# Performance work log

Measured on AMD Instinct MI355X. Metric: run time of the kernel, lower is better.

## Reference

```python
import jax, jax.numpy as jnp
import numpy as np

N = 50000   # nodes
E = 600000  # edges
D = 128     # in = hidden = out channels (must be equal per the cat/mean readout)
B = 4096    # number of lookup indices


def setup_inputs() -> dict:
    key = jax.random.key(0)
    ks = jax.random.split(key, 8)
    x = jax.random.normal(ks[0], (N, D), dtype=jnp.float32)
    edge_index = jax.random.randint(ks[1], (2, E), 0, N)
    edge_weight = jax.random.uniform(ks[2], (E,), dtype=jnp.float32)
    inputs_idx = jax.random.randint(ks[3], (B,), 0, N + 1)  # N is the appended zero row
    def lin_w(k, din, dout):
        return jax.random.normal(k, (din, dout), dtype=jnp.float32) / np.sqrt(din).astype(np.float32)
    W1 = lin_w(ks[4], D, D); b1 = jnp.zeros((D,), jnp.float32)
    W2 = lin_w(ks[5], D, D); b2 = jnp.zeros((D,), jnp.float32)
    W3 = lin_w(ks[6], D, D); b3 = jnp.zeros((D,), jnp.float32)
    return {"inputs_idx": inputs_idx, "x": x, "edge_index": edge_index,
            "edge_weight": edge_weight, "W1": W1, "b1": b1, "W2": W2,
            "b2": b2, "W3": W3, "b3": b3}


def gcn_conv(x, W, b, src, dst, w):
    # PyG GCNConv with add_self_loops=True (fill weight 1) and symmetric norm.
    deg = jnp.zeros((N,), x.dtype).at[dst].add(w) + 1.0  # self-loop contributes 1
    dinv = jax.lax.rsqrt(deg)
    norm = dinv[src] * w * dinv[dst]                      # [E]
    h = x @ W                                             # [N, D]
    agg = jax.ops.segment_sum(norm[:, None] * h[src], dst, num_segments=N)
    agg = agg + h * (dinv * dinv)[:, None]                # self-loop term: deg^-1 * h
    return agg + b


def lookup(x, inputs_idx):
    # append a zero row, then gather
    x_ = jnp.concatenate([x, jnp.zeros((1, x.shape[-1]), x.dtype)], axis=0)
    return x_[inputs_idx]  # [B, D]


def reference(inputs_idx, x, edge_index, edge_weight, W1, b1, W2, b2, W3, b3):
    src, dst = edge_index[0], edge_index[1]
    x1 = jax.nn.relu(gcn_conv(x, W1, b1, src, dst, edge_weight))
    x2 = jax.nn.relu(gcn_conv(x1, W2, b2, src, dst, edge_weight))
    x3 = jax.nn.relu(gcn_conv(x2, W3, b3, src, dst, edge_weight))
    e1 = lookup(x1, inputs_idx)
    e2 = lookup(x2, inputs_idx)
    e3 = lookup(x3, inputs_idx)
    # torch.cat([1,B,D]x3, dim=0).mean(0) == elementwise mean of the three
    return (e1 + e2 + e3) / 3.0
```

## Files before the change

### kernel.cpp

```cpp
#include <hip/hip_runtime.h>
#include <hip/hip_fp16.h>

#define D 128
#define STRIDE 48

typedef _Float16 f16x8 __attribute__((ext_vector_type(8)));
typedef float f32x4 __attribute__((ext_vector_type(4)));
struct h4 { __half2 a, b; };

__global__ __launch_bounds__(256) void zero_kernel(int* __restrict__ p, int n) {
  int i = blockIdx.x * 256 + threadIdx.x;
  if (i < n) p[i] = 0;
}

__global__ __launch_bounds__(256) void build_kernel(
    const int* __restrict__ ei, const float* __restrict__ ew,
    int* __restrict__ cnt, int2* __restrict__ pairs, int E) {
  int e = blockIdx.x * 256 + threadIdx.x;
  if (e >= E) return;
  int s = ei[e], d = ei[E + e];
  int rank = atomicAdd(&cnt[d], 1);
  if (rank < STRIDE) pairs[(size_t)d * STRIDE + rank] = make_int2(s, __float_as_int(ew[e]));
}

__global__ __launch_bounds__(256) void deg_dinv_kernel(
    int* __restrict__ cnt, const int2* __restrict__ pairs,
    float* __restrict__ dinv, int N) {
  int n = blockIdx.x * 4 + (threadIdx.x >> 6);
  int lane = threadIdx.x & 63;
  if (n >= N) return;
  int c = cnt[n];
  c = c < STRIDE ? c : STRIDE;
  float v = (lane < c) ? __int_as_float(pairs[(size_t)n * STRIDE + lane].y) : 0.f;
#pragma unroll
  for (int o = 32; o > 0; o >>= 1) v += __shfl_xor(v, o, 64);
  if (lane == 0) {
    dinv[n] = rsqrtf(v + 1.0f);
    cnt[n] = c;
  }
}

__global__ __launch_bounds__(256) void norm_kernel(
    const int* __restrict__ cnt, const float* __restrict__ dinv,
    int2* __restrict__ pairs, int N) {
  int n = blockIdx.x * 4 + (threadIdx.x >> 6);
  int lane = threadIdx.x & 63;
  if (n >= N) return;
  int c = cnt[n];
  float di = dinv[n];
  if (lane < c) {
    int2 p = pairs[(size_t)n * STRIDE + lane];
    p.y = __float_as_int(dinv[p.x] * __int_as_float(p.y) * di);
    pairs[(size_t)n * STRIDE + lane] = p;
  }
}

__global__ __launch_bounds__(256) void tohalf_kernel(
    const float* __restrict__ in, __half* __restrict__ out, int n4) {
  int t = blockIdx.x * 256 + threadIdx.x;
  if (t >= n4) return;
  float4 v = ((const float4*)in)[t];
  h4 o = {__floats2half2_rn(v.x, v.y), __floats2half2_rn(v.z, v.w)};
  ((h4*)out)[t] = o;
}

__global__ __launch_bounds__(256) void wtrans_kernel(
    const float* __restrict__ W1, const float* __restrict__ W2,
    const float* __restrict__ W3, __half* __restrict__ WT1,
    __half* __restrict__ WT2, __half* __restrict__ WT3) {
  int t = blockIdx.x * 256 + threadIdx.x;
  if (t >= 3 * D * D) return;
  int m = t >> 14;
  int i = t & (D * D - 1);
  int k = i >> 7, n = i & 127;
  const float* W = (m == 0) ? W1 : (m == 1) ? W2 : W3;
  __half* WT = (m == 0) ? WT1 : (m == 1) ? WT2 : WT3;
  WT[n * D + k] = __float2half(W[k * D + n]);
}

__global__ __launch_bounds__(256) void agg_kernel(
    const __half* __restrict__ x16, const float* __restrict__ dinv,
    const int* __restrict__ cnt, const int2* __restrict__ pairs,
    __half* __restrict__ agg16, int N) {
  int gw = (blockIdx.x * 256 + threadIdx.x) >> 6;
  int lane = threadIdx.x & 63;
  if (gw >= N) return;
  const __half2* xs = (const __half2*)x16;
  float di = dinv[gw];
  int c = cnt[gw];
  const int2* pr = pairs + (size_t)gw * STRIDE;
  float2 acc = __half22float2(xs[(size_t)gw * 64 + lane]);
  acc.x *= di * di;
  acc.y *= di * di;
  int e = 0;
  for (; e + 4 <= c; e += 4) {
    int2 p0 = pr[e], p1 = pr[e + 1], p2 = pr[e + 2], p3 = pr[e + 3];
    float n0 = __int_as_float(p0.y), n1 = __int_as_float(p1.y);
    float n2 = __int_as_float(p2.y), n3 = __int_as_float(p3.y);
    float2 v0 = __half22float2(xs[(size_t)p0.x * 64 + lane]);
    float2 v1 = __half22float2(xs[(size_t)p1.x * 64 + lane]);
    float2 v2 = __half22float2(xs[(size_t)p2.x * 64 + lane]);
    float2 v3 = __half22float2(xs[(size_t)p3.x * 64 + lane]);
    acc.x += n0 * v0.x + n1 * v1.x + n2 * v2.x + n3 * v3.x;
    acc.y += n0 * v0.y + n1 * v1.y + n2 * v2.y + n3 * v3.y;
  }
  for (; e < c; e++) {
    int2 p0 = pr[e];
    float n0 = __int_as_float(p0.y);
    float2 v0 = __half22float2(xs[(size_t)p0.x * 64 + lane]);
    acc.x += n0 * v0.x;
    acc.y += n0 * v0.y;
  }
  ((__half2*)agg16)[(size_t)gw * 64 + lane] = __floats2half2_rn(acc.x, acc.y);
}

__global__ __launch_bounds__(256) void agg_idx_kernel(
    const __half* __restrict__ x16, const float* __restrict__ dinv,
    const int* __restrict__ cnt, const int2* __restrict__ pairs,
    const int* __restrict__ idx, __half* __restrict__ aggI, int B, int N) {
  int gw = (blockIdx.x * 256 + threadIdx.x) >> 6;
  int lane = threadIdx.x & 63;
  if (gw >= B) return;
  const __half2* xs = (const __half2*)x16;
  float2 acc = make_float2(0.f, 0.f);
  int node = idx[gw];
  if ((unsigned)node < (unsigned)N) {
    float di = dinv[node];
    int c = cnt[node];
    const int2* pr = pairs + (size_t)node * STRIDE;
    acc = __half22float2(xs[(size_t)node * 64 + lane]);
    acc.x *= di * di;
    acc.y *= di * di;
    int e = 0;
    for (; e + 4 <= c; e += 4) {
      int2 p0 = pr[e], p1 = pr[e + 1], p2 = pr[e + 2], p3 = pr[e + 3];
      float n0 = __int_as_float(p0.y), n1 = __int_as_float(p1.y);
      float n2 = __int_as_float(p2.y), n3 = __int_as_float(p3.y);
      float2 v0 = __half22float2(xs[(size_t)p0.x * 64 + lane]);
      float2 v1 = __half22float2(xs[(size_t)p1.x * 64 + lane]);
      float2 v2 = __half22float2(xs[(size_t)p2.x * 64 + lane]);
      float2 v3 = __half22float2(xs[(size_t)p3.x * 64 + lane]);
      acc.x += n0 * v0.x + n1 * v1.x + n2 * v2.x + n3 * v3.x;
      acc.y += n0 * v0.y + n1 * v1.y + n2 * v2.y + n3 * v3.y;
    }
    for (; e < c; e++) {
      int2 p0 = pr[e];
      float n0 = __int_as_float(p0.y);
      float2 v0 = __half22float2(xs[(size_t)p0.x * 64 + lane]);
      acc.x += n0 * v0.x;
      acc.y += n0 * v0.y;
    }
  }
  ((__half2*)aggI)[(size_t)gw * 64 + lane] = __floats2half2_rn(acc.x, acc.y);
}

__global__ __launch_bounds__(256) void gemm16(
    const __half* __restrict__ A16, const __half* __restrict__ WT,
    const float* __restrict__ bias, __half* __restrict__ out16, int n) {
  __shared__ __half Bs[D * D];
  const int tid = threadIdx.x;
  const int wid = tid >> 6;
  const int lane = tid & 63;
  const int l15 = lane & 15;
  const int lk = lane >> 4;
  const int rbase = blockIdx.x * 128 + wid * 32;

  f16x8 a[2][4];
#pragma unroll
  for (int m = 0; m < 2; m++) {
    int r = rbase + m * 16 + l15;
    bool ok = (r < n);
    const __half* arow = A16 + (size_t)r * D + lk * 8;
#pragma unroll
    for (int kk = 0; kk < 4; kk++) {
      f16x8 z = {0, 0, 0, 0, 0, 0, 0, 0};
      a[m][kk] = ok ? *(const f16x8*)(arow + kk * 32) : z;
    }
  }
  {
    const int4* src = (const int4*)WT;
#pragma unroll
    for (int i = 0; i < 8; i++) {
      int slot = tid + i * 256;
      int byte = slot << 4;
      int row = byte >> 8;
      int4 v = src[slot];
      *(int4*)((char*)Bs + (byte ^ ((row & 7) << 4))) = v;
    }
  }
  __syncthreads();

  f32x4 c[2][8];
#pragma unroll
  for (int m = 0; m < 2; m++)
#pragma unroll
    for (int nf = 0; nf < 8; nf++) c[m][nf] = (f32x4){0.f, 0.f, 0.f, 0.f};

#pragma unroll
  for (int kk = 0; kk < 4; kk++) {
#pragma unroll
    for (int nf = 0; nf < 8; nf++) {
      int byte = ((nf * 16 + l15) << 8) + (kk << 6) + (lk << 4);
      byte ^= (l15 & 7) << 4;
      f16x8 b = *(const f16x8*)((const char*)Bs + byte);
      c[0][nf] = __builtin_amdgcn_mfma_f32_16x16x32_f16(a[0][kk], b, c[0][nf], 0, 0, 0);
      c[1][nf] = __builtin_amdgcn_mfma_f32_16x16x32_f16(a[1][kk], b, c[1][nf], 0, 0, 0);
    }
  }

#pragma unroll
  for (int nf = 0; nf < 8; nf++) {
    float bv = bias[nf * 16 + l15];
#pragma unroll
    for (int m = 0; m < 2; m++) {
      int r0 = rbase + m * 16 + lk * 4;
#pragma unroll
      for (int rg = 0; rg < 4; rg++) {
        int r = r0 + rg;
        if (r < n) {
          float v = fmaxf(c[m][nf][rg] + bv, 0.f);
          out16[(size_t)r * D + nf * 16 + l15] = __float2half(v);
        }
      }
    }
  }
}

__global__ __launch_bounds__(256) void combine_kernel(
    const __half* __restrict__ oA, const __half* __restrict__ oB,
    const __half* __restrict__ oC, const int* __restrict__ idx,
    float* __restrict__ out, int B, int N) {
  int t = blockIdx.x * 256 + threadIdx.x;
  if (t >= B * 16) return;
  int b = t >> 4, c8 = t & 15;
  int id = idx[b];
  float4 p0 = make_float4(0.f, 0.f, 0.f, 0.f);
  float4 p1 = make_float4(0.f, 0.f, 0.f, 0.f);
  if ((unsigned)id < (unsigned)N) {
    int4 r1 = *(const int4*)(oA + (size_t)id * D + c8 * 8);
    int4 r2 = *(const int4*)(oB + (size_t)id * D + c8 * 8);
    int4 r3 = *(const int4*)(oC + (size_t)b * D + c8 * 8);
    const __half2 *h1 = (const __half2*)&r1, *h2 = (const __half2*)&r2,
                  *h3 = (const __half2*)&r3;
#pragma unroll
    for (int j = 0; j < 4; j++) {
      float2 f1 = __half22float2(h1[j]);
      float2 f2 = __half22float2(h2[j]);
      float2 f3 = __half22float2(h3[j]);
      float sx = (f1.x + f2.x + f3.x) * (1.0f / 3.0f);
      float sy = (f1.y + f2.y + f3.y) * (1.0f / 3.0f);
      if (j < 2) { ((float*)&p0)[j * 2] = sx; ((float*)&p0)[j * 2 + 1] = sy; }
      else       { ((float*)&p1)[(j - 2) * 2] = sx; ((float*)&p1)[(j - 2) * 2 + 1] = sy; }
    }
  }
  float* op = out + (size_t)b * D + c8 * 8;
  *(float4*)op = p0;
  *(float4*)(op + 4) = p1;
}


extern "C" void kernel_launch(void* const* d_in, const int* in_sizes, int n_in,
                              void* d_out, int out_size, void* d_ws, size_t ws_size,
                              hipStream_t stream) {
  const int*   inputs_idx  = (const int*)d_in[0];
  const float* x           = (const float*)d_in[1];
  const int*   edge_index  = (const int*)d_in[2];
  const float* edge_weight = (const float*)d_in[3];
  const float* W1 = (const float*)d_in[4];
  const float* b1 = (const float*)d_in[5];
  const float* W2 = (const float*)d_in[6];
  const float* b2 = (const float*)d_in[7];
  const float* W3 = (const float*)d_in[8];
  const float* b3 = (const float*)d_in[9];
  float* out = (float*)d_out;

  const int B = in_sizes[0];
  const int N = in_sizes[1] / D;
  const int E = in_sizes[3];
  (void)n_in; (void)out_size; (void)ws_size;

  char* p = (char*)d_ws;
  size_t off = 0;
  auto alloc = [&](size_t bytes) -> void* {
    void* r = p + off;
    off += (bytes + 255) & ~(size_t)255;
    return r;
  };
  int*    cnt   = (int*)alloc((size_t)N * 4);
  float*  dinv  = (float*)alloc((size_t)N * 4);
  int2*   pairs = (int2*)alloc((size_t)N * STRIDE * 8);
  __half* x16   = (__half*)alloc((size_t)N * D * 2);
  __half* aggT  = (__half*)alloc((size_t)N * D * 2);
  __half* oA    = (__half*)alloc((size_t)N * D * 2);
  __half* oB    = (__half*)alloc((size_t)N * D * 2);
  __half* oC    = (__half*)alloc((size_t)B * D * 2);
  __half* WT1   = (__half*)alloc((size_t)D * D * 2);
  __half* WT2   = (__half*)alloc((size_t)D * D * 2);
  __half* WT3   = (__half*)alloc((size_t)D * D * 2);

  int eb = (E + 255) / 256;
  int wb = (N + 3) / 4;
  zero_kernel<<<(N + 255) / 256, 256, 0, stream>>>(cnt, N);
  build_kernel<<<eb, 256, 0, stream>>>(edge_index, edge_weight, cnt, pairs, E);
  deg_dinv_kernel<<<wb, 256, 0, stream>>>(cnt, pairs, dinv, N);
  norm_kernel<<<wb, 256, 0, stream>>>(cnt, dinv, pairs, N);
  tohalf_kernel<<<(N * 32 + 255) / 256, 256, 0, stream>>>(x, x16, N * 32);
  wtrans_kernel<<<(3 * D * D + 255) / 256, 256, 0, stream>>>(W1, W2, W3, WT1, WT2, WT3);

  int ab = (N + 3) / 4;
  int gb = (N + 127) / 128;
  int lb = (B * 16 + 255) / 256;

  agg_kernel<<<ab, 256, 0, stream>>>(x16, dinv, cnt, pairs, aggT, N);
  gemm16<<<gb, 256, 0, stream>>>(aggT, WT1, b1, oA, N);
  agg_kernel<<<ab, 256, 0, stream>>>(oA, dinv, cnt, pairs, aggT, N);
  gemm16<<<gb, 256, 0, stream>>>(aggT, WT2, b2, oB, N);
  int ib = (B + 3) / 4;
  int gb3 = (B + 127) / 128;
  agg_idx_kernel<<<ib, 256, 0, stream>>>(oB, dinv, cnt, pairs, inputs_idx, aggT, B, N);
  gemm16<<<gb3, 256, 0, stream>>>(aggT, WT3, b3, oC, B);
  combine_kernel<<<lb, 256, 0, stream>>>(oA, oB, oC, inputs_idx, out, B, N);
}
```

Baseline: 186.7 us.

## Compute layer-2 only for lookup nodes and their neighbors via compacted list

Marks the lookup nodes and their direct in-neighbors, compacts them into a list with an inverse map, and runs the second-layer aggregation and GEMM only over that subset. Layer 3 and the final combine then read layer-2 outputs through the inverse map. The GEMM tile is also halved to 64 rows per block so the smaller, dynamically sized workload spreads over more blocks. This adds mark and compact kernels, atomics and an indirect lookup, and launches a full-size grid that exits early past the device-side count.

```diff
diff --git a/kernel.cpp b/kernel.cpp
--- a/kernel.cpp
+++ b/kernel.cpp
@@ -76,6 +76,31 @@
   const float* W = (m == 0) ? W1 : (m == 1) ? W2 : W3;
   __half* WT = (m == 0) ? WT1 : (m == 1) ? WT2 : WT3;
   WT[n * D + k] = __float2half(W[k * D + n]);
+}
+
+__global__ __launch_bounds__(256) void mark_kernel(
+    const int* __restrict__ idx, const int* __restrict__ cnt,
+    const int2* __restrict__ pairs, int* __restrict__ flags, int B, int N) {
+  int b = (blockIdx.x * 256 + threadIdx.x) >> 6;
+  int lane = threadIdx.x & 63;
+  if (b >= B) return;
+  int id = idx[b];
+  if ((unsigned)id >= (unsigned)N) return;
+  if (lane == 0) flags[id] = 1;
+  int c = cnt[id];
+  if (lane < c) flags[pairs[(size_t)id * STRIDE + lane].x] = 1;
+}
+
+__global__ __launch_bounds__(256) void compact_kernel(
+    const int* __restrict__ flags, int* __restrict__ list,
+    int* __restrict__ invmap, int* __restrict__ cntr, int N) {
+  int i = blockIdx.x * 256 + threadIdx.x;
+  if (i >= N) return;
+  if (flags[i]) {
+    int pos = atomicAdd(cntr, 1);
+    list[pos] = i;
+    invmap[i] = pos;
+  }
 }
 
 __global__ __launch_bounds__(256) void agg_kernel(
@@ -114,39 +139,79 @@
   ((__half2*)agg16)[(size_t)gw * 64 + lane] = __floats2half2_rn(acc.x, acc.y);
 }
 
-__global__ __launch_bounds__(256) void agg_idx_kernel(
+__global__ __launch_bounds__(256) void agg_list_kernel(
     const __half* __restrict__ x16, const float* __restrict__ dinv,
     const int* __restrict__ cnt, const int2* __restrict__ pairs,
-    const int* __restrict__ idx, __half* __restrict__ aggI, int B, int N) {
+    const int* __restrict__ list, const int* __restrict__ Mp,
+    __half* __restrict__ aggO) {
   int gw = (blockIdx.x * 256 + threadIdx.x) >> 6;
   int lane = threadIdx.x & 63;
+  if (gw >= *Mp) return;
+  int node = list[gw];
+  const __half2* xs = (const __half2*)x16;
+  float di = dinv[node];
+  int c = cnt[node];
+  const int2* pr = pairs + (size_t)node * STRIDE;
+  float2 acc = __half22float2(xs[(size_t)node * 64 + lane]);
+  acc.x *= di * di;
+  acc.y *= di * di;
+  int e = 0;
+  for (; e + 4 <= c; e += 4) {
+    int2 p0 = pr[e], p1 = pr[e + 1], p2 = pr[e + 2], p3 = pr[e + 3];
+    float n0 = __int_as_float(p0.y), n1 = __int_as_float(p1.y);
+    float n2 = __int_as_float(p2.y), n3 = __int_as_float(p3.y);
+    float2 v0 = __half22float2(xs[(size_t)p0.x * 64 + lane]);
+    float2 v1 = __half22float2(xs[(size_t)p1.x * 64 + lane]);
+    float2 v2 = __half22float2(xs[(size_t)p2.x * 64 + lane]);
+    float2 v3 = __half22float2(xs[(size_t)p3.x * 64 + lane]);
+    acc.x += n0 * v0.x + n1 * v1.x + n2 * v2.x + n3 * v3.x;
+    acc.y += n0 * v0.y + n1 * v1.y + n2 * v2.y + n3 * v3.y;
+  }
+  for (; e < c; e++) {
+    int2 p0 = pr[e];
+    float n0 = __int_as_float(p0.y);
+    float2 v0 = __half22float2(xs[(size_t)p0.x * 64 + lane]);
+    acc.x += n0 * v0.x;
+    acc.y += n0 * v0.y;
+  }
+  ((__half2*)aggO)[(size_t)gw * 64 + lane] = __floats2half2_rn(acc.x, acc.y);
+}
+
+__global__ __launch_bounds__(256) void agg_idx3_kernel(
+    const __half* __restrict__ x16c, const float* __restrict__ dinv,
+    const int* __restrict__ cnt, const int2* __restrict__ pairs,
+    const int* __restrict__ idx, const int* __restrict__ invmap,
+    __half* __restrict__ aggI, int B, int N) {
+  int gw = (blockIdx.x * 256 + threadIdx.x) >> 6;
+  int lane = threadIdx.x & 63;
   if (gw >= B) return;
-  const __half2* xs = (const __half2*)x16;
+  const __half2* xs = (const __half2*)x16c;
   float2 acc = make_float2(0.f, 0.f);
   int node = idx[gw];
   if ((unsigned)node < (unsigned)N) {
     float di = dinv[node];
     int c = cnt[node];
     const int2* pr = pairs + (size_t)node * STRIDE;
-    acc = __half22float2(xs[(size_t)node * 64 + lane]);
+    acc = __half22float2(xs[(size_t)invmap[node] * 64 + lane]);
     acc.x *= di * di;
     acc.y *= di * di;
     int e = 0;
     for (; e + 4 <= c; e += 4) {
       int2 p0 = pr[e], p1 = pr[e + 1], p2 = pr[e + 2], p3 = pr[e + 3];
+      int j0 = invmap[p0.x], j1 = invmap[p1.x], j2 = invmap[p2.x], j3 = invmap[p3.x];
       float n0 = __int_as_float(p0.y), n1 = __int_as_float(p1.y);
       float n2 = __int_as_float(p2.y), n3 = __int_as_float(p3.y);
-      float2 v0 = __half22float2(xs[(size_t)p0.x * 64 + lane]);
-      float2 v1 = __half22float2(xs[(size_t)p1.x * 64 + lane]);
-      float2 v2 = __half22float2(xs[(size_t)p2.x * 64 + lane]);
-      float2 v3 = __half22float2(xs[(size_t)p3.x * 64 + lane]);
+      float2 v0 = __half22float2(xs[(size_t)j0 * 64 + lane]);
+      float2 v1 = __half22float2(xs[(size_t)j1 * 64 + lane]);
+      float2 v2 = __half22float2(xs[(size_t)j2 * 64 + lane]);
+      float2 v3 = __half22float2(xs[(size_t)j3 * 64 + lane]);
       acc.x += n0 * v0.x + n1 * v1.x + n2 * v2.x + n3 * v3.x;
       acc.y += n0 * v0.y + n1 * v1.y + n2 * v2.y + n3 * v3.y;
     }
     for (; e < c; e++) {
       int2 p0 = pr[e];
       float n0 = __int_as_float(p0.y);
-      float2 v0 = __half22float2(xs[(size_t)p0.x * 64 + lane]);
+      float2 v0 = __half22float2(xs[(size_t)invmap[p0.x] * 64 + lane]);
       acc.x += n0 * v0.x;
       acc.y += n0 * v0.y;
     }
@@ -156,25 +221,27 @@
 
 __global__ __launch_bounds__(256) void gemm16(
     const __half* __restrict__ A16, const __half* __restrict__ WT,
-    const float* __restrict__ bias, __half* __restrict__ out16, int n) {
+    const float* __restrict__ bias, __half* __restrict__ out16, int n,
+    const int* __restrict__ np) {
+  if (np) n = *np;
+  if (blockIdx.x * 64 >= n) return;
   __shared__ __half Bs[D * D];
   const int tid = threadIdx.x;
   const int wid = tid >> 6;
   const int lane = tid & 63;
   const int l15 = lane & 15;
   const int lk = lane >> 4;
-  const int rbase = blockIdx.x * 128 + wid * 32;
-
-  f16x8 a[2][4];
-#pragma unroll
-  for (int m = 0; m < 2; m++) {
-    int r = rbase + m * 16 + l15;
+  const int rbase = blockIdx.x * 64 + wid * 16;
+
+  f16x8 a[4];
+  {
+    int r = rbase + l15;
     bool ok = (r < n);
     const __half* arow = A16 + (size_t)r * D + lk * 8;
 #pragma unroll
     for (int kk = 0; kk < 4; kk++) {
       f16x8 z = {0, 0, 0, 0, 0, 0, 0, 0};
-      a[m][kk] = ok ? *(const f16x8*)(arow + kk * 32) : z;
+      a[kk] = ok ? *(const f16x8*)(arow + kk * 32) : z;
     }
   }
   {
@@ -190,11 +257,9 @@
   }
   __syncthreads();
 
-  f32x4 c[2][8];
-#pragma unroll
-  for (int m = 0; m < 2; m++)
-#pragma unroll
-    for (int nf = 0; nf < 8; nf++) c[m][nf] = (f32x4){0.f, 0.f, 0.f, 0.f};
+  f32x4 c[8];
+#pragma unroll
+  for (int nf = 0; nf < 8; nf++) c[nf] = (f32x4){0.f, 0.f, 0.f, 0.f};
 
 #pragma unroll
   for (int kk = 0; kk < 4; kk++) {
@@ -203,33 +268,29 @@
       int byte = ((nf * 16 + l15) << 8) + (kk << 6) + (lk << 4);
       byte ^= (l15 & 7) << 4;
       f16x8 b = *(const f16x8*)((const char*)Bs + byte);
-      c[0][nf] = __builtin_amdgcn_mfma_f32_16x16x32_f16(a[0][kk], b, c[0][nf], 0, 0, 0);
-      c[1][nf] = __builtin_amdgcn_mfma_f32_16x16x32_f16(a[1][kk], b, c[1][nf], 0, 0, 0);
+      c[nf] = __builtin_amdgcn_mfma_f32_16x16x32_f16(a[kk], b, c[nf], 0, 0, 0);
     }
   }
 
 #pragma unroll
   for (int nf = 0; nf < 8; nf++) {
     float bv = bias[nf * 16 + l15];
-#pragma unroll
-    for (int m = 0; m < 2; m++) {
-      int r0 = rbase + m * 16 + lk * 4;
-#pragma unroll
-      for (int rg = 0; rg < 4; rg++) {
-        int r = r0 + rg;
-        if (r < n) {
-          float v = fmaxf(c[m][nf][rg] + bv, 0.f);
-          out16[(size_t)r * D + nf * 16 + l15] = __float2half(v);
-        }
+    int r0 = rbase + lk * 4;
+#pragma unroll
+    for (int rg = 0; rg < 4; rg++) {
+      int r = r0 + rg;
+      if (r < n) {
+        float v = fmaxf(c[nf][rg] + bv, 0.f);
+        out16[(size_t)r * D + nf * 16 + l15] = __float2half(v);
       }
     }
   }
 }
 
 __global__ __launch_bounds__(256) void combine_kernel(
-    const __half* __restrict__ oA, const __half* __restrict__ oB,
+    const __half* __restrict__ oA, const __half* __restrict__ oBc,
     const __half* __restrict__ oC, const int* __restrict__ idx,
-    float* __restrict__ out, int B, int N) {
+    const int* __restrict__ invmap, float* __restrict__ out, int B, int N) {
   int t = blockIdx.x * 256 + threadIdx.x;
   if (t >= B * 16) return;
   int b = t >> 4, c8 = t & 15;
@@ -237,21 +298,23 @@
   float4 p0 = make_float4(0.f, 0.f, 0.f, 0.f);
   float4 p1 = make_float4(0.f, 0.f, 0.f, 0.f);
   if ((unsigned)id < (unsigned)N) {
+    int j = invmap[id];
     int4 r1 = *(const int4*)(oA + (size_t)id * D + c8 * 8);
-    int4 r2 = *(const int4*)(oB + (size_t)id * D + c8 * 8);
+    int4 r2 = *(const int4*)(oBc + (size_t)j * D + c8 * 8);
     int4 r3 = *(const int4*)(oC + (size_t)b * D + c8 * 8);
     const __half2 *h1 = (const __half2*)&r1, *h2 = (const __half2*)&r2,
                   *h3 = (const __half2*)&r3;
-#pragma unroll
-    for (int j = 0; j < 4; j++) {
-      float2 f1 = __half22float2(h1[j]);
-      float2 f2 = __half22float2(h2[j]);
-      float2 f3 = __half22float2(h3[j]);
-      float sx = (f1.x + f2.x + f3.x) * (1.0f / 3.0f);
-      float sy = (f1.y + f2.y + f3.y) * (1.0f / 3.0f);
-      if (j < 2) { ((float*)&p0)[j * 2] = sx; ((float*)&p0)[j * 2 + 1] = sy; }
-      else       { ((float*)&p1)[(j - 2) * 2] = sx; ((float*)&p1)[(j - 2) * 2 + 1] = sy; }
-    }
+    float o[8];
+#pragma unroll
+    for (int j2 = 0; j2 < 4; j2++) {
+      float2 f1 = __half22float2(h1[j2]);
+      float2 f2 = __half22float2(h2[j2]);
+      float2 f3 = __half22float2(h3[j2]);
+      o[j2 * 2]     = (f1.x + f2.x + f3.x) * (1.0f / 3.0f);
+      o[j2 * 2 + 1] = (f1.y + f2.y + f3.y) * (1.0f / 3.0f);
+    }
+    p0 = make_float4(o[0], o[1], o[2], o[3]);
+    p1 = make_float4(o[4], o[5], o[6], o[7]);
   }
   float* op = out + (size_t)b * D + c8 * 8;
   *(float4*)op = p0;
@@ -286,13 +349,18 @@
     off += (bytes + 255) & ~(size_t)255;
     return r;
   };
-  int*    cnt   = (int*)alloc((size_t)N * 4);
+  int*    iblk  = (int*)alloc(((size_t)2 * N + 64) * 4);
+  int*    cnt   = iblk;
+  int*    flags = iblk + N;
+  int*    cntr  = iblk + 2 * N;
   float*  dinv  = (float*)alloc((size_t)N * 4);
   int2*   pairs = (int2*)alloc((size_t)N * STRIDE * 8);
+  int*    list  = (int*)alloc((size_t)N * 4);
+  int*    invmap= (int*)alloc((size_t)N * 4);
   __half* x16   = (__half*)alloc((size_t)N * D * 2);
   __half* aggT  = (__half*)alloc((size_t)N * D * 2);
   __half* oA    = (__half*)alloc((size_t)N * D * 2);
-  __half* oB    = (__half*)alloc((size_t)N * D * 2);
+  __half* oBc   = (__half*)alloc((size_t)N * D * 2);
   __half* oC    = (__half*)alloc((size_t)B * D * 2);
   __half* WT1   = (__half*)alloc((size_t)D * D * 2);
   __half* WT2   = (__half*)alloc((size_t)D * D * 2);
@@ -300,24 +368,27 @@
 
   int eb = (E + 255) / 256;
   int wb = (N + 3) / 4;
-  zero_kernel<<<(N + 255) / 256, 256, 0, stream>>>(cnt, N);
+  zero_kernel<<<(2 * N + 1 + 255) / 256, 256, 0, stream>>>(iblk, 2 * N + 1);
   build_kernel<<<eb, 256, 0, stream>>>(edge_index, edge_weight, cnt, pairs, E);
   deg_dinv_kernel<<<wb, 256, 0, stream>>>(cnt, pairs, dinv, N);
   norm_kernel<<<wb, 256, 0, stream>>>(cnt, dinv, pairs, N);
   tohalf_kernel<<<(N * 32 + 255) / 256, 256, 0, stream>>>(x, x16, N * 32);
   wtrans_kernel<<<(3 * D * D + 255) / 256, 256, 0, stream>>>(W1, W2, W3, WT1, WT2, WT3);
+  mark_kernel<<<(B + 3) / 4, 256, 0, stream>>>(inputs_idx, cnt, pairs, flags, B, N);
+  compact_kernel<<<(N + 255) / 256, 256, 0, stream>>>(flags, list, invmap, cntr, N);
 
   int ab = (N + 3) / 4;
-  int gb = (N + 127) / 128;
+  int gb = (N + 63) / 64;
   int lb = (B * 16 + 255) / 256;
+  int ib = (B + 3) / 4;
+  int gb3 = (B + 63) / 64;
 
   agg_kernel<<<ab, 256, 0, stream>>>(x16, dinv, cnt, pairs, aggT, N);
-  gemm16<<<gb, 256, 0, stream>>>(aggT, WT1, b1, oA, N);
-  agg_kernel<<<ab, 256, 0, stream>>>(oA, dinv, cnt, pairs, aggT, N);
-  gemm16<<<gb, 256, 0, stream>>>(aggT, WT2, b2, oB, N);
-  int ib = (B + 3) / 4;
-  int gb3 = (B + 127) / 128;
-  agg_idx_kernel<<<ib, 256, 0, stream>>>(oB, dinv, cnt, pairs, inputs_idx, aggT, B, N);
-  gemm16<<<gb3, 256, 0, stream>>>(aggT, WT3, b3, oC, B);
-  combine_kernel<<<lb, 256, 0, stream>>>(oA, oB, oC, inputs_idx, out, B, N);
-}
+  gemm16<<<gb, 256, 0, stream>>>(aggT, WT1, b1, oA, N, nullptr);
+  agg_list_kernel<<<ab, 256, 0, stream>>>(oA, dinv, cnt, pairs, list, cntr, aggT);
+  gemm16<<<gb, 256, 0, stream>>>(aggT, WT2, b2, oBc, N, cntr);
+  agg_idx3_kernel<<<ib, 256, 0, stream>>>(oBc, dinv, cnt, pairs, inputs_idx,
+                                          invmap, aggT, B, N);
+  gemm16<<<gb3, 256, 0, stream>>>(aggT, WT3, b3, oC, B, nullptr);
+  combine_kernel<<<lb, 256, 0, stream>>>(oA, oBc, oC, inputs_idx, invmap, out, B, N);
+}
```

After: 178.2 us (median of 2 runs). 1.05x faster.
